# Kernel optimization log

Hardware: AMD Instinct MI355X
Metric: run time of the kernel (lower is better)

The kernel has to match this reference:

```python
import jax, jax.numpy as jnp
import numpy as np

B = 256        # graphs (documents) per batch
NPG = 200      # nodes per graph
EPG = 1600     # edges per graph (~2*ngram+2 per token)
D = 200        # hidden_size_node (glove.6B.200d)
V = 50000      # vocab size
ENUM = 2000000 # global edge-id vocabulary
C = 20         # class_num
N = B * NPG
E = B * EPG


def setup_inputs() -> dict:
    key = jax.random.key(0)
    ks = jax.random.split(key, 8)
    node_ids = jax.random.randint(ks[0], (N,), 0, V, dtype=jnp.int32)
    # graph-local endpoints + per-graph node offset (mimics dgl.batch)
    src_local = jax.random.randint(ks[1], (E,), 0, NPG, dtype=jnp.int32)
    dst_local = jax.random.randint(ks[2], (E,), 0, NPG, dtype=jnp.int32)
    off = jnp.repeat(jnp.arange(B, dtype=jnp.int32) * NPG, EPG)
    edge_src = src_local + off
    edge_dst = dst_local + off
    edge_ids = jax.random.randint(ks[3], (E,), 0, ENUM, dtype=jnp.int32)
    node_seg = jnp.repeat(jnp.arange(B, dtype=jnp.int32), NPG)
    node_emb = jax.random.normal(ks[4], (V, D), dtype=jnp.float32) * 0.1
    # trainable_edges=True -> edge weight table initialized to ones
    edge_w = jnp.ones((ENUM, 1), dtype=jnp.float32)
    W = jax.random.normal(ks[5], (D, C), dtype=jnp.float32) * 0.05
    b = jnp.zeros((C,), dtype=jnp.float32)
    return {"node_emb": node_emb, "edge_w": edge_w, "W": W, "b": b,
            "node_ids": node_ids, "edge_src": edge_src, "edge_dst": edge_dst,
            "edge_ids": edge_ids, "node_seg": node_seg}


def reference(node_emb, edge_w, W, b, node_ids, edge_src, edge_dst, edge_ids, node_seg):
    h = node_emb[node_ids]                       # [N, D] node hidden states
    msg = h[edge_src] * edge_w[edge_ids]         # [E, D] src feat * edge weight
    # scatter-max reduce onto destination nodes (dgl max reduce)
    h_max = jax.ops.segment_max(msg, edge_dst, num_segments=N)
    h_max = jnp.where(jnp.isfinite(h_max), h_max, jnp.float32(0.0))  # empty segs -> 0 like DGL
    pooled = jax.ops.segment_sum(h_max, node_seg, num_segments=B)   # dgl.sum_nodes -> [B, D]
    # dropout is identity in eval / p=0.0
    return jax.nn.relu(pooled) @ W + b           # [B, C]
```

## Files before the change

kernel.cpp:

```cpp
#include <hip/hip_runtime.h>

#define NPG 200
#define EPG 1600
#define DIM 200
#define NCLS 20
#define THREADS 1024
#define NWAVES 16
#define Q4 50
#define NROWU 100
#define NCHUNK (NPG * Q4)
#define NEG_INF (-__builtin_inff())

__global__ __launch_bounds__(THREADS, 4) void gnn_fused(
    const float* __restrict__ node_emb,
    const float* __restrict__ edge_w,
    const float* __restrict__ Wm,
    const float* __restrict__ bv,
    const int*   __restrict__ node_ids,
    const int*   __restrict__ edge_src,
    const int*   __restrict__ edge_dst,
    const int*   __restrict__ edge_ids,
    float*       __restrict__ out)
{
    __shared__ unsigned       rows[NPG * NROWU];
    __shared__ uint2          ce[EPG];
    __shared__ int            nidrow[NPG];
    __shared__ unsigned short srcl[EPG];
    __shared__ unsigned short dstl[EPG];
    __shared__ float          wv[EPG];
    __shared__ int            csum[256];
    __shared__ int            cursor[NPG];
    __shared__ short          wstart[NWAVES + 1];
    __shared__ float          part[NWAVES][DIM];
    __shared__ float          pooled[DIM];

    const int g       = blockIdx.x;
    const int tid     = threadIdx.x;
    const int gbase_n = g * NPG;
    const int gbase_e = g * EPG;

    if (tid < NPG) nidrow[tid] = node_ids[gbase_n + tid];
    if (tid < 256) csum[tid] = 0;
    __syncthreads();

    for (int e = tid; e < EPG; e += THREADS) {
        int s = edge_src[gbase_e + e] - gbase_n;
        int d = edge_dst[gbase_e + e] - gbase_n;
        srcl[e] = (unsigned short)s;
        dstl[e] = (unsigned short)d;
        wv[e]   = edge_w[edge_ids[gbase_e + e]];
        atomicAdd(&csum[d], 1);
    }

    for (int i = tid; i < NCHUNK; i += THREADS) {
        const int row = i / Q4;
        const int c   = i - row * Q4;
        const float4 v = *reinterpret_cast<const float4*>(
            node_emb + (size_t)nidrow[row] * DIM + c * 4);
        const unsigned b0 = ((__float_as_uint(v.y) + 0x8000u) & 0xffff0000u) |
                            ((__float_as_uint(v.x) + 0x8000u) >> 16);
        const unsigned b1 = ((__float_as_uint(v.w) + 0x8000u) & 0xffff0000u) |
                            ((__float_as_uint(v.z) + 0x8000u) >> 16);
        *reinterpret_cast<uint2*>(&rows[row * NROWU + c * 2]) = make_uint2(b0, b1);
    }
    __syncthreads();

    if (tid < 64) {
        int4 cc = *reinterpret_cast<int4*>(&csum[tid * 4]);
        int s1 = cc.x + cc.y, s2 = s1 + cc.z, s3 = s2 + cc.w;
        int carry = s3;
        #pragma unroll
        for (int off = 1; off < 64; off <<= 1) {
            int t = __shfl_up(carry, off);
            if (tid >= off) carry += t;
        }
        const int base = carry - s3;
        int4 o; o.x = base + cc.x; o.y = base + s1; o.z = base + s2; o.w = base + s3;
        *reinterpret_cast<int4*>(&csum[tid * 4]) = o;
    }
    __syncthreads();

    if (tid < NPG) cursor[tid] = (tid == 0) ? 0 : csum[tid - 1];
    if (tid <= NWAVES) {
        int target = tid * (EPG / NWAVES);
        int lo = 0, hi = NPG;
        while (lo < hi) {
            int mid = (lo + hi) >> 1;
            int excl = (mid == 0) ? 0 : csum[mid - 1];
            if (excl >= target) hi = mid; else lo = mid + 1;
        }
        wstart[tid] = (short)lo;
    }
    __syncthreads();

    for (int e = tid; e < EPG; e += THREADS) {
        int d    = dstl[e];
        int excl = (d == 0) ? 0 : csum[d - 1];
        int pos  = atomicAdd(&cursor[d], 1);
        unsigned pack = (unsigned)srcl[e] * 200u | (pos == excl ? 1u : 0u);
        ce[pos] = make_uint2(pack, __float_as_uint(wv[e]));
    }
    __syncthreads();

    const int w    = tid >> 6;
    const int lane = tid & 63;
    if (lane < Q4) {
        const int n0 = wstart[w];
        const int n1 = wstart[w + 1];
        const int kb = (n0 == 0) ? 0 : csum[n0 - 1];
        const int ke = (n1 == 0) ? 0 : csum[n1 - 1];
        const int lane2 = lane * 2;

        float4 p = make_float4(0.f, 0.f, 0.f, 0.f);
        float4 m = make_float4(0.f, 0.f, 0.f, 0.f);

        #pragma unroll 8
        for (int k = kb; k < ke; ++k) {
            const uint2 q2  = ce[k];
            const bool  ns  = (q2.x & 1u);
            const float wgt = __uint_as_float(q2.y);
            const uint2 rv  = *reinterpret_cast<const uint2*>(&rows[(q2.x >> 1) + lane2]);
            const float c0 = __uint_as_float(rv.x << 16)         * wgt;
            const float c1 = __uint_as_float(rv.x & 0xffff0000u) * wgt;
            const float c2 = __uint_as_float(rv.y << 16)         * wgt;
            const float c3 = __uint_as_float(rv.y & 0xffff0000u) * wgt;
            p.x += ns ? m.x : 0.0f;  p.y += ns ? m.y : 0.0f;
            p.z += ns ? m.z : 0.0f;  p.w += ns ? m.w : 0.0f;
            m.x = fmaxf(ns ? NEG_INF : m.x, c0);
            m.y = fmaxf(ns ? NEG_INF : m.y, c1);
            m.z = fmaxf(ns ? NEG_INF : m.z, c2);
            m.w = fmaxf(ns ? NEG_INF : m.w, c3);
        }
        p.x += m.x; p.y += m.y; p.z += m.z; p.w += m.w;
        *reinterpret_cast<float4*>(&part[w][lane * 4]) = p;
    }
    __syncthreads();

    if (tid < DIM) {
        float t = 0.f;
        #pragma unroll
        for (int i = 0; i < NWAVES; ++i) t += part[i][tid];
        pooled[tid] = fmaxf(t, 0.0f);
    }
    __syncthreads();

    if (tid < NCLS) {
        float acc = bv[tid];
        #pragma unroll 4
        for (int k = 0; k < DIM; ++k)
            acc += pooled[k] * Wm[k * NCLS + tid];
        out[g * NCLS + tid] = acc;
    }
}

extern "C" void kernel_launch(void* const* d_in, const int* in_sizes, int n_in,
                              void* d_out, int out_size, void* d_ws, size_t ws_size,
                              hipStream_t stream) {
    const float* node_emb = (const float*)d_in[0];
    const float* edge_w   = (const float*)d_in[1];
    const float* Wm       = (const float*)d_in[2];
    const float* bv       = (const float*)d_in[3];
    const int*   node_ids = (const int*)d_in[4];
    const int*   edge_src = (const int*)d_in[5];
    const int*   edge_dst = (const int*)d_in[6];
    const int*   edge_ids = (const int*)d_in[7];

    const int N = in_sizes[4];
    const int B = N / NPG;

    gnn_fused<<<B, THREADS, 0, stream>>>(node_emb, edge_w, Wm, bv,
                                         node_ids, edge_src, edge_dst, edge_ids,
                                         (float*)d_out);
}
```

Measured before the change: 131.9 us.

## Split each graph across two blocks and gather embeddings directly from global memory

Each graph is now handled by two blocks, each owning half of the destination nodes. The bf16 staging of all 200 embedding rows into shared memory is dropped, and the max-reduce loop instead reads fp32 float4 rows straight from node_emb through precomputed byte offsets. A second small kernel sums the two partial poolings, applies ReLU and runs the classifier with W staged in shared memory. This roughly halves per-block shared memory and doubles the block count for more occupancy, at the cost of redundant edge-list reads per half, scattered global loads in the inner loop, and an extra launch plus a workspace round trip.

After: 126.5 us. 4.1% less time.

```diff
diff --git a/kernel.cpp b/kernel.cpp
--- a/kernel.cpp
+++ b/kernel.cpp
@@ -4,89 +4,80 @@
 #define EPG 1600
 #define DIM 200
 #define NCLS 20
+#define NGRAPH 256
 #define THREADS 1024
 #define NWAVES 16
+#define NPB 100
 #define Q4 50
-#define NROWU 100
-#define NCHUNK (NPG * Q4)
 #define NEG_INF (-__builtin_inff())
 
-__global__ __launch_bounds__(THREADS, 4) void gnn_fused(
+__global__ __launch_bounds__(THREADS, 8) void gnn_gather(
     const float* __restrict__ node_emb,
     const float* __restrict__ edge_w,
-    const float* __restrict__ Wm,
-    const float* __restrict__ bv,
     const int*   __restrict__ node_ids,
     const int*   __restrict__ edge_src,
     const int*   __restrict__ edge_dst,
     const int*   __restrict__ edge_ids,
-    float*       __restrict__ out)
+    float*       __restrict__ partial)
 {
-    __shared__ unsigned       rows[NPG * NROWU];
-    __shared__ uint2          ce[EPG];
-    __shared__ int            nidrow[NPG];
+    __shared__ int            nidb[NPG];
     __shared__ unsigned short srcl[EPG];
     __shared__ unsigned short dstl[EPG];
     __shared__ float          wv[EPG];
-    __shared__ int            csum[256];
-    __shared__ int            cursor[NPG];
+    __shared__ uint2          ce[EPG];
+    __shared__ int            csum[128];
+    __shared__ int            cursor[NPB];
     __shared__ short          wstart[NWAVES + 1];
     __shared__ float          part[NWAVES][DIM];
-    __shared__ float          pooled[DIM];
 
-    const int g       = blockIdx.x;
-    const int tid     = threadIdx.x;
+    const int bid = blockIdx.x;
+    const int g   = bid & (NGRAPH - 1);
+    const int h   = bid >> 8;
+    const int n0g = h * NPB;
+    const int tid = threadIdx.x;
     const int gbase_n = g * NPG;
     const int gbase_e = g * EPG;
 
-    if (tid < NPG) nidrow[tid] = node_ids[gbase_n + tid];
-    if (tid < 256) csum[tid] = 0;
+    if (tid < NPG) nidb[tid] = node_ids[gbase_n + tid] * (DIM * 4);
+    if (tid < 128) csum[tid] = 0;
     __syncthreads();
 
     for (int e = tid; e < EPG; e += THREADS) {
-        int s = edge_src[gbase_e + e] - gbase_n;
-        int d = edge_dst[gbase_e + e] - gbase_n;
+        int s  = edge_src[gbase_e + e] - gbase_n;
+        int dl = edge_dst[gbase_e + e] - gbase_n;
         srcl[e] = (unsigned short)s;
-        dstl[e] = (unsigned short)d;
-        wv[e]   = edge_w[edge_ids[gbase_e + e]];
-        atomicAdd(&csum[d], 1);
-    }
-
-    for (int i = tid; i < NCHUNK; i += THREADS) {
-        const int row = i / Q4;
-        const int c   = i - row * Q4;
-        const float4 v = *reinterpret_cast<const float4*>(
-            node_emb + (size_t)nidrow[row] * DIM + c * 4);
-        const unsigned b0 = ((__float_as_uint(v.y) + 0x8000u) & 0xffff0000u) |
-                            ((__float_as_uint(v.x) + 0x8000u) >> 16);
-        const unsigned b1 = ((__float_as_uint(v.w) + 0x8000u) & 0xffff0000u) |
-                            ((__float_as_uint(v.z) + 0x8000u) >> 16);
-        *reinterpret_cast<uint2*>(&rows[row * NROWU + c * 2]) = make_uint2(b0, b1);
+        dstl[e] = (unsigned short)dl;
+        int n = dl - n0g;
+        if ((unsigned)n < NPB) {
+            wv[e] = edge_w[edge_ids[gbase_e + e]];
+            atomicAdd(&csum[n], 1);
+        }
     }
     __syncthreads();
 
     if (tid < 64) {
-        int4 cc = *reinterpret_cast<int4*>(&csum[tid * 4]);
-        int s1 = cc.x + cc.y, s2 = s1 + cc.z, s3 = s2 + cc.w;
-        int carry = s3;
+        int2 c = *reinterpret_cast<int2*>(&csum[tid * 2]);
+        int s1 = c.x + c.y;
+        int carry = s1;
         #pragma unroll
         for (int off = 1; off < 64; off <<= 1) {
             int t = __shfl_up(carry, off);
             if (tid >= off) carry += t;
         }
-        const int base = carry - s3;
-        int4 o; o.x = base + cc.x; o.y = base + s1; o.z = base + s2; o.w = base + s3;
-        *reinterpret_cast<int4*>(&csum[tid * 4]) = o;
+        int base = carry - s1;
+        int2 o; o.x = base + c.x; o.y = base + s1;
+        *reinterpret_cast<int2*>(&csum[tid * 2]) = o;
     }
     __syncthreads();
 
-    if (tid < NPG) cursor[tid] = (tid == 0) ? 0 : csum[tid - 1];
+    const int total = csum[NPB - 1];
+    if (tid < NPB) cursor[tid] = (tid == 0) ? 0 : csum[tid - 1];
     if (tid <= NWAVES) {
-        int target = tid * (EPG / NWAVES);
-        int lo = 0, hi = NPG;
+        int target = (tid * total) >> 4;
+        int lo = 0, hi = NPB;
         while (lo < hi) {
             int mid = (lo + hi) >> 1;
-            int excl = (mid == 0) ? 0 : csum[mid - 1];
+            int excl = mid ? csum[mid - 1] : 0;
             if (excl >= target) hi = mid; else lo = mid + 1;
         }
         wstart[tid] = (short)lo;
@@ -94,22 +85,24 @@
     __syncthreads();
 
     for (int e = tid; e < EPG; e += THREADS) {
-        int d    = dstl[e];
-        int excl = (d == 0) ? 0 : csum[d - 1];
-        int pos  = atomicAdd(&cursor[d], 1);
-        unsigned pack = (unsigned)srcl[e] * 200u | (pos == excl ? 1u : 0u);
-        ce[pos] = make_uint2(pack, __float_as_uint(wv[e]));
+        int n = (int)dstl[e] - n0g;
+        if ((unsigned)n < NPB) {
+            int excl = n ? csum[n - 1] : 0;
+            int pos  = atomicAdd(&cursor[n], 1);
+            unsigned pack = (unsigned)nidb[srcl[e]] | (pos == excl ? 1u : 0u);
+            ce[pos] = make_uint2(pack, __float_as_uint(wv[e]));
+        }
     }
     __syncthreads();
 
     const int w    = tid >> 6;
     const int lane = tid & 63;
     if (lane < Q4) {
-        const int n0 = wstart[w];
-        const int n1 = wstart[w + 1];
-        const int kb = (n0 == 0) ? 0 : csum[n0 - 1];
-        const int ke = (n1 == 0) ? 0 : csum[n1 - 1];
-        const int lane2 = lane * 2;
+        const int a0 = wstart[w];
+        const int a1 = wstart[w + 1];
+        const int kb = a0 ? csum[a0 - 1] : 0;
+        const int ke = a1 ? csum[a1 - 1] : 0;
+        const char* lb = (const char*)node_emb + lane * 16;
 
         float4 p = make_float4(0.f, 0.f, 0.f, 0.f);
         float4 m = make_float4(0.f, 0.f, 0.f, 0.f);
@@ -119,17 +112,13 @@
             const uint2 q2  = ce[k];
             const bool  ns  = (q2.x & 1u);
             const float wgt = __uint_as_float(q2.y);
-            const uint2 rv  = *reinterpret_cast<const uint2*>(&rows[(q2.x >> 1) + lane2]);
-            const float c0 = __uint_as_float(rv.x << 16)         * wgt;
-            const float c1 = __uint_as_float(rv.x & 0xffff0000u) * wgt;
-            const float c2 = __uint_as_float(rv.y << 16)         * wgt;
-            const float c3 = __uint_as_float(rv.y & 0xffff0000u) * wgt;
+            const float4 v  = *reinterpret_cast<const float4*>(lb + (q2.x & ~1u));
             p.x += ns ? m.x : 0.0f;  p.y += ns ? m.y : 0.0f;
             p.z += ns ? m.z : 0.0f;  p.w += ns ? m.w : 0.0f;
-            m.x = fmaxf(ns ? NEG_INF : m.x, c0);
-            m.y = fmaxf(ns ? NEG_INF : m.y, c1);
-            m.z = fmaxf(ns ? NEG_INF : m.z, c2);
-            m.w = fmaxf(ns ? NEG_INF : m.w, c3);
+            m.x = fmaxf(ns ? NEG_INF : m.x, v.x * wgt);
+            m.y = fmaxf(ns ? NEG_INF : m.y, v.y * wgt);
+            m.z = fmaxf(ns ? NEG_INF : m.z, v.z * wgt);
+            m.w = fmaxf(ns ? NEG_INF : m.w, v.w * wgt);
         }
         p.x += m.x; p.y += m.y; p.z += m.z; p.w += m.w;
         *reinterpret_cast<float4*>(&part[w][lane * 4]) = p;
@@ -140,7 +129,25 @@
         float t = 0.f;
         #pragma unroll
         for (int i = 0; i < NWAVES; ++i) t += part[i][tid];
-        pooled[tid] = fmaxf(t, 0.0f);
+        partial[(h * NGRAPH + g) * DIM + tid] = t;
+    }
+}
+
+__global__ __launch_bounds__(256) void gnn_head(
+    const float* __restrict__ partial,
+    const float* __restrict__ Wm,
+    const float* __restrict__ bv,
+    float*       __restrict__ out)
+{
+    __shared__ float pooled[DIM];
+    __shared__ float Ws[DIM * NCLS];
+    const int g   = blockIdx.x;
+    const int tid = threadIdx.x;
+
+    for (int i = tid; i < DIM * NCLS; i += 256) Ws[i] = Wm[i];
+    if (tid < DIM) {
+        float s = partial[g * DIM + tid] + partial[(NGRAPH + g) * DIM + tid];
+        pooled[tid] = fmaxf(s, 0.0f);
     }
     __syncthreads();
 
@@ -148,7 +155,7 @@
         float acc = bv[tid];
         #pragma unroll 4
         for (int k = 0; k < DIM; ++k)
-            acc += pooled[k] * Wm[k * NCLS + tid];
+            acc += pooled[k] * Ws[k * NCLS + tid];
         out[g * NCLS + tid] = acc;
     }
 }
@@ -165,10 +172,10 @@
     const int*   edge_dst = (const int*)d_in[6];
     const int*   edge_ids = (const int*)d_in[7];
 
-    const int N = in_sizes[4];
-    const int B = N / NPG;
+    float* partial = (float*)d_ws;
 
-    gnn_fused<<<B, THREADS, 0, stream>>>(node_emb, edge_w, Wm, bv,
-                                         node_ids, edge_src, edge_dst, edge_ids,
-                                         (float*)d_out);
+    gnn_gather<<<2 * NGRAPH, THREADS, 0, stream>>>(node_emb, edge_w,
+                                                   node_ids, edge_src, edge_dst, edge_ids,
+                                                   partial);
+    gnn_head<<<NGRAPH, 256, 0, stream>>>(partial, Wm, bv, (float*)d_out);
 }
```

## Split gather and edge staging across half-blocks, use nested per-node max loop

Applied to the files above, without the earlier changes.

The first half of the block now gathers and converts the embedding rows while the second half loads edges into a packed shared-memory list and counts destinations, so the two phases run concurrently. The per-edge segment-start flag and select logic are replaced by an outer loop over nodes with an inner max loop, giving simpler inner-loop arithmetic at the cost of irregular inner trip counts. The src offset is prescaled to a byte offset, and launch_bounds drops the min-blocks hint, which may change register allocation.

Measured after the change: 131.2 us. About the same (-0.5%).

```diff
diff --git a/kernel.cpp b/kernel.cpp
--- a/kernel.cpp
+++ b/kernel.cpp
@@ -4,14 +4,13 @@
 #define EPG 1600
 #define DIM 200
 #define NCLS 20
+#define NGRAPH 256
 #define THREADS 1024
 #define NWAVES 16
+#define ROWU 100
 #define Q4 50
-#define NROWU 100
-#define NCHUNK (NPG * Q4)
-#define NEG_INF (-__builtin_inff())
 
-__global__ __launch_bounds__(THREADS, 4) void gnn_fused(
+__global__ __launch_bounds__(THREADS) void gnn_fused(
     const float* __restrict__ node_emb,
     const float* __restrict__ edge_w,
     const float* __restrict__ Wm,
@@ -22,46 +21,44 @@
     const int*   __restrict__ edge_ids,
     float*       __restrict__ out)
 {
-    __shared__ unsigned       rows[NPG * NROWU];
-    __shared__ uint2          ce[EPG];
-    __shared__ int            nidrow[NPG];
-    __shared__ unsigned short srcl[EPG];
-    __shared__ unsigned short dstl[EPG];
-    __shared__ float          wv[EPG];
-    __shared__ int            csum[256];
-    __shared__ int            cursor[NPG];
-    __shared__ short          wstart[NWAVES + 1];
-    __shared__ float          part[NWAVES][DIM];
-    __shared__ float          pooled[DIM];
+    __shared__ unsigned rows[NPG * ROWU];
+    __shared__ uint2    elist[EPG];
+    __shared__ uint2    ce[EPG];
+    __shared__ int      csum[256];
+    __shared__ int      cursor[NPG];
+    __shared__ short    wstart[NWAVES + 1];
+    __shared__ float    part[NWAVES][DIM];
+    __shared__ float    pooled[DIM];
 
     const int g       = blockIdx.x;
     const int tid     = threadIdx.x;
     const int gbase_n = g * NPG;
     const int gbase_e = g * EPG;
 
-    if (tid < NPG) nidrow[tid] = node_ids[gbase_n + tid];
     if (tid < 256) csum[tid] = 0;
     __syncthreads();
 
-    for (int e = tid; e < EPG; e += THREADS) {
-        int s = edge_src[gbase_e + e] - gbase_n;
-        int d = edge_dst[gbase_e + e] - gbase_n;
-        srcl[e] = (unsigned short)s;
-        dstl[e] = (unsigned short)d;
-        wv[e]   = edge_w[edge_ids[gbase_e + e]];
-        atomicAdd(&csum[d], 1);
-    }
-
-    for (int i = tid; i < NCHUNK; i += THREADS) {
-        const int row = i / Q4;
-        const int c   = i - row * Q4;
-        const float4 v = *reinterpret_cast<const float4*>(
-            node_emb + (size_t)nidrow[row] * DIM + c * 4);
-        const unsigned b0 = ((__float_as_uint(v.y) + 0x8000u) & 0xffff0000u) |
-                            ((__float_as_uint(v.x) + 0x8000u) >> 16);
-        const unsigned b1 = ((__float_as_uint(v.w) + 0x8000u) & 0xffff0000u) |
-                            ((__float_as_uint(v.z) + 0x8000u) >> 16);
-        *reinterpret_cast<uint2*>(&rows[row * NROWU + c * 2]) = make_uint2(b0, b1);
+    if (tid < 512) {
+        for (int i = tid; i < NPG * Q4; i += 512) {
+            const int n = i / Q4;
+            const int c = i - n * Q4;
+            const float4 v = *reinterpret_cast<const float4*>(
+                node_emb + (size_t)node_ids[gbase_n + n] * DIM + c * 4);
+            const unsigned b0 = ((__float_as_uint(v.y) + 0x8000u) & 0xffff0000u) |
+                                ((__float_as_uint(v.x) + 0x8000u) >> 16);
+            const unsigned b1 = ((__float_as_uint(v.w) + 0x8000u) & 0xffff0000u) |
+                                ((__float_as_uint(v.z) + 0x8000u) >> 16);
+            *reinterpret_cast<uint2*>(&rows[n * ROWU + c * 2]) = make_uint2(b0, b1);
+        }
+    } else {
+        for (int e = tid - 512; e < EPG; e += 512) {
+            const int   s  = edge_src[gbase_e + e] - gbase_n;
+            const int   dl = edge_dst[gbase_e + e] - gbase_n;
+            const float wv = edge_w[edge_ids[gbase_e + e]];
+            elist[e] = make_uint2((unsigned)s | ((unsigned)dl << 16),
+                                  __float_as_uint(wv));
+            atomicAdd(&csum[dl], 1);
+        }
     }
     __syncthreads();
 
@@ -80,58 +77,57 @@
     }
     __syncthreads();
 
-    if (tid < NPG) cursor[tid] = (tid == 0) ? 0 : csum[tid - 1];
-    if (tid <= NWAVES) {
-        int target = tid * (EPG / NWAVES);
+    if (tid < NPG) cursor[tid] = tid ? csum[tid - 1] : 0;
+    if (tid >= 256 && tid <= 256 + NWAVES) {
+        const int t  = tid - 256;
+        int target = t * (EPG / NWAVES);
         int lo = 0, hi = NPG;
         while (lo < hi) {
             int mid = (lo + hi) >> 1;
-            int excl = (mid == 0) ? 0 : csum[mid - 1];
+            int excl = mid ? csum[mid - 1] : 0;
             if (excl >= target) hi = mid; else lo = mid + 1;
         }
-        wstart[tid] = (short)lo;
+        wstart[t] = (short)lo;
     }
     __syncthreads();
 
     for (int e = tid; e < EPG; e += THREADS) {
-        int d    = dstl[e];
-        int excl = (d == 0) ? 0 : csum[d - 1];
-        int pos  = atomicAdd(&cursor[d], 1);
-        unsigned pack = (unsigned)srcl[e] * 200u | (pos == excl ? 1u : 0u);
-        ce[pos] = make_uint2(pack, __float_as_uint(wv[e]));
+        const uint2 m  = elist[e];
+        const int   dl = m.x >> 16;
+        const int   pos = atomicAdd(&cursor[dl], 1);
+        ce[pos] = make_uint2((m.x & 0xffffu) * 400u, m.y);
     }
     __syncthreads();
 
     const int w    = tid >> 6;
     const int lane = tid & 63;
     if (lane < Q4) {
-        const int n0 = wstart[w];
-        const int n1 = wstart[w + 1];
-        const int kb = (n0 == 0) ? 0 : csum[n0 - 1];
-        const int ke = (n1 == 0) ? 0 : csum[n1 - 1];
-        const int lane2 = lane * 2;
-
+        const char* rb = (const char*)rows + lane * 8;
         float4 p = make_float4(0.f, 0.f, 0.f, 0.f);
-        float4 m = make_float4(0.f, 0.f, 0.f, 0.f);
-
-        #pragma unroll 8
-        for (int k = kb; k < ke; ++k) {
-            const uint2 q2  = ce[k];
-            const bool  ns  = (q2.x & 1u);
-            const float wgt = __uint_as_float(q2.y);
-            const uint2 rv  = *reinterpret_cast<const uint2*>(&rows[(q2.x >> 1) + lane2]);
-            const float c0 = __uint_as_float(rv.x << 16)         * wgt;
-            const float c1 = __uint_as_float(rv.x & 0xffff0000u) * wgt;
-            const float c2 = __uint_as_float(rv.y << 16)         * wgt;
-            const float c3 = __uint_as_float(rv.y & 0xffff0000u) * wgt;
-            p.x += ns ? m.x : 0.0f;  p.y += ns ? m.y : 0.0f;
-            p.z += ns ? m.z : 0.0f;  p.w += ns ? m.w : 0.0f;
-            m.x = fmaxf(ns ? NEG_INF : m.x, c0);
-            m.y = fmaxf(ns ? NEG_INF : m.y, c1);
-            m.z = fmaxf(ns ? NEG_INF : m.z, c2);
-            m.w = fmaxf(ns ? NEG_INF : m.w, c3);
+        const int a0 = wstart[w], a1 = wstart[w + 1];
+        for (int n = a0; n < a1; ++n) {
+            int k = n ? csum[n - 1] : 0;
+            const int ke = csum[n];
+            if (k >= ke) continue;
+            uint2 q  = ce[k];
+            uint2 rv = *reinterpret_cast<const uint2*>(rb + q.x);
+            float wgt = __uint_as_float(q.y);
+            float4 m;
+            m.x = __uint_as_float(rv.x << 16)          * wgt;
+            m.y = __uint_as_float(rv.x & 0xffff0000u)  * wgt;
+            m.z = __uint_as_float(rv.y << 16)          * wgt;
+            m.w = __uint_as_float(rv.y & 0xffff0000u)  * wgt;
+            for (++k; k < ke; ++k) {
+                q   = ce[k];
+                rv  = *reinterpret_cast<const uint2*>(rb + q.x);
+                wgt = __uint_as_float(q.y);
+                m.x = fmaxf(m.x, __uint_as_float(rv.x << 16)         * wgt);
+                m.y = fmaxf(m.y, __uint_as_float(rv.x & 0xffff0000u) * wgt);
+                m.z = fmaxf(m.z, __uint_as_float(rv.y << 16)         * wgt);
+                m.w = fmaxf(m.w, __uint_as_float(rv.y & 0xffff0000u) * wgt);
+            }
+            p.x += m.x; p.y += m.y; p.z += m.z; p.w += m.w;
         }
-        p.x += m.x; p.y += m.y; p.z += m.z; p.w += m.w;
         *reinterpret_cast<float4*>(&part[w][lane * 4]) = p;
     }
     __syncthreads();
```
